# Kernel optimization log

Hardware: AMD Instinct MI355X
Metric: run time of the kernel (lower is better)

## Reference

```python
import jax, jax.numpy as jnp
import numpy as np

T, B, A, H = 1024, 16, 8, 256


def setup_inputs() -> dict:
    key = jax.random.key(0)
    ks = jax.random.split(key, 8)
    s = 1.0 / np.sqrt(H)  # approximate lecun/orthogonal scale for stability
    return {
        "ins": jax.random.normal(ks[0], (T, B, A, H), dtype=jnp.float32),
        "resets": jax.random.randint(ks[1], (T, B, A), 0, 2) == 1,
        "h0": jnp.zeros((B, A, H), dtype=jnp.float32),
        "W_ir": jax.random.normal(ks[2], (H, H), dtype=jnp.float32) * s,
        "W_iz": jax.random.normal(ks[3], (H, H), dtype=jnp.float32) * s,
        "W_in": jax.random.normal(ks[4], (H, H), dtype=jnp.float32) * s,
        "b_ir": jnp.zeros((H,), dtype=jnp.float32),
        "b_iz": jnp.zeros((H,), dtype=jnp.float32),
        "b_in": jnp.zeros((H,), dtype=jnp.float32),
        "W_hr": jax.random.normal(ks[5], (H, H), dtype=jnp.float32) * s,
        "W_hz": jax.random.normal(ks[6], (H, H), dtype=jnp.float32) * s,
        "W_hn": jax.random.normal(ks[7], (H, H), dtype=jnp.float32) * s,
        "b_hn": jnp.zeros((H,), dtype=jnp.float32),
    }


def reference(ins, resets, h0, W_ir, W_iz, W_in, b_ir, b_iz, b_in, W_hr, W_hz, W_hn, b_hn):
    # Precompute the input-side gate projections for all timesteps at once
    # (mathematically identical to flax GRUCell's per-step dense_i calls).
    xr = ins @ W_ir + b_ir  # [T, B, A, H]
    xz = ins @ W_iz + b_iz
    xn = ins @ W_in + b_in

    def step(h, xs):
        xr_t, xz_t, xn_t, rst_t = xs
        # reset masking: re-init carry to zeros where episode resets
        h = jnp.where(rst_t[..., None], jnp.zeros_like(h), h)
        r = jax.nn.sigmoid(xr_t + h @ W_hr)
        z = jax.nn.sigmoid(xz_t + h @ W_hz)
        n = jnp.tanh(xn_t + r * (h @ W_hn + b_hn))
        new_h = (1.0 - z) * n + z * h
        return new_h, new_h

    final_h, ys = jax.lax.scan(step, h0, (xr, xz, xn, resets))
    return ys  # [T, B, A, H]; final carry == ys[-1]
```

## Files before the change

### kernel.cpp

```cpp
#include <hip/hip_runtime.h>

#define BA 128
#define H 256
#define TH 768
#define NROWS (1024 * BA)
#define LCAP 65536
#define NBUCK 8
#define MT 32
#define AP 264

typedef _Float16 h2_t __attribute__((ext_vector_type(2)));
typedef _Float16 h8_t __attribute__((ext_vector_type(8)));
typedef short s8_t __attribute__((ext_vector_type(8)));
typedef float f4_t __attribute__((ext_vector_type(4)));
typedef unsigned short u16;
typedef u16 us4_t __attribute__((ext_vector_type(4)));
typedef unsigned int u32;
typedef u32 v64u __attribute__((ext_vector_type(64)));

__device__ __forceinline__ float bf2f(u16 u) {
  union { u32 i; float f; } c; c.i = ((u32)u) << 16; return c.f;
}
__device__ __forceinline__ u16 f2bf(float f) {
  union { float f; u32 i; } c; c.f = f;
  u32 r = c.i + 0x7FFFu + ((c.i >> 16) & 1u);
  return (u16)(r >> 16);
}
__device__ __forceinline__ float sigm(float x) {
  float e = __builtin_amdgcn_exp2f(-x * 1.442695040888963f);
  return __builtin_amdgcn_rcpf(1.0f + e);
}
__device__ __forceinline__ float tanh_(float x) {
  float e = __builtin_amdgcn_exp2f(x * 2.885390081777927f);
  return 1.0f - 2.0f * __builtin_amdgcn_rcpf(1.0f + e);
}
__device__ __forceinline__ float ldf(const void* p, bool f32, size_t idx) {
  return f32 ? ((const float*)p)[idx] : bf2f(((const u16*)p)[idx]);
}
__device__ __forceinline__ int ldrst(const void* p, bool isbyte, size_t idx) {
  return isbyte ? (int)((const unsigned char*)p)[idx] : ((const int*)p)[idx];
}
__device__ __forceinline__ float F2(h2_t a, h2_t b, float c) {
#if defined(__has_builtin) && __has_builtin(__builtin_amdgcn_fdot2)
  return __builtin_amdgcn_fdot2(a, b, c, false);
#else
  return c + (float)a[0] * (float)b[0] + (float)a[1] * (float)b[1];
#endif
}

__global__ __launch_bounds__(256) void kdetect(const u32* __restrict__ insw,
                                               const u32* __restrict__ rstw,
                                               const u32* __restrict__ whrw,
                                               const u32* __restrict__ wirw,
                                               int* __restrict__ flags,
                                               int* __restrict__ cnt) {
  __shared__ int c0, c1, c2, c3;
  if (threadIdx.x == 0) { c0 = 0; c1 = 0; c2 = 0; c3 = 0; }
  if (threadIdx.x < NBUCK) cnt[threadIdx.x] = 0;
  __syncthreads();
  if (!(fabsf(bf2f((u16)(insw[threadIdx.x] & 0xFFFFu))) < 1e10f)) atomicAdd(&c0, 1);
  if (!(fabsf(bf2f((u16)(whrw[threadIdx.x] & 0xFFFFu))) < 1e10f)) atomicAdd(&c2, 1);
  if (!(fabsf(bf2f((u16)(wirw[threadIdx.x] & 0xFFFFu))) < 1e10f)) atomicAdd(&c3, 1);
  if (threadIdx.x < 128 && rstw[threadIdx.x] > 1u) atomicAdd(&c1, 1);
  __syncthreads();
  if (threadIdx.x == 0) {
    flags[0] = (c0 > 8) ? 1 : 0;
    flags[1] = (c1 > 0) ? 1 : 0;
    flags[2] = (c2 > 8) ? 1 : 0;
    flags[3] = (c3 > 8) ? 1 : 0;
  }
}

__global__ __launch_bounds__(256) void kprep(const void* __restrict__ ins,
                                             u16* __restrict__ insb,
                                             const int* __restrict__ flags) {
  bool f32in = flags[0] != 0;
  size_t i0 = ((size_t)blockIdx.x * 256 + threadIdx.x) * 8;
  s8_t v;
  if (f32in) {
    f4_t x0 = *(const f4_t*)((const float*)ins + i0);
    f4_t x1 = *(const f4_t*)((const float*)ins + i0 + 4);
#pragma unroll
    for (int i = 0; i < 4; ++i) v[i] = (short)f2bf(x0[i]);
#pragma unroll
    for (int i = 0; i < 4; ++i) v[4 + i] = (short)f2bf(x1[i]);
  } else {
    v = *(const s8_t*)((const u16*)ins + i0);
  }
  *(s8_t*)(insb + i0) = v;
}

__global__ __launch_bounds__(256) void ktrans(const void* __restrict__ W0, const void* __restrict__ W1,
                                              const void* __restrict__ W2, const void* __restrict__ W3,
                                              const void* __restrict__ W4, const void* __restrict__ W5,
                                              u16* __restrict__ WT, const int* __restrict__ flags) {
  __shared__ u16 tile[64][65];
  int g = blockIdx.z;
  bool f32in = ((g < 3) ? flags[3] : flags[2]) != 0;
  bool toF16 = (g >= 3);
  const void* srcs[6] = {W0, W1, W2, W3, W4, W5};
  const void* src = srcs[g];
  int k0 = blockIdx.x * 64, j0 = blockIdx.y * 64;
  int tid = threadIdx.x;
#pragma unroll
  for (int p = 0; p < 16; ++p) {
    int e = p * 256 + tid;
    int kr = e >> 6, jc = e & 63;
    size_t idx = (size_t)(k0 + kr) * H + j0 + jc;
    float v = f32in ? ((const float*)src)[idx] : bf2f(((const u16*)src)[idx]);
    u16 bits;
    if (toF16) {
      _Float16 h = (_Float16)v;
      bits = __builtin_bit_cast(u16, h);
    } else {
      bits = f2bf(v);
    }
    tile[kr][jc] = bits;
  }
  __syncthreads();
  u16* dst = WT + (size_t)g * H * H;
#pragma unroll
  for (int p = 0; p < 16; ++p) {
    int e = p * 256 + tid;
    int jr = e >> 6, kc = e & 63;
    dst[(size_t)(j0 + jr) * H + k0 + kc] = tile[kc][jr];
  }
}

__global__ __launch_bounds__(256) void kswz(const u16* __restrict__ WT, u16* __restrict__ WhB) {
  int f = blockIdx.x * 256 + threadIdx.x;
  if (f >= 8 * 48 * 64) return;
  int lane = f & 63;
  int cg = (f >> 6) % 48;
  int kk = (f >> 6) / 48;
  int g = cg >> 4;
  int col = ((cg & 15) << 4) + (lane & 15);
  int k0 = kk * 32 + ((lane >> 4) << 3);
  const u16* src = WT + (size_t)(3 + g) * H * H + (size_t)col * H + k0;
  *(s8_t*)(WhB + (size_t)f * 8) = *(const s8_t*)src;
}

#define LDK 40
__global__ __launch_bounds__(256) void kgemm(const void* __restrict__ ins,
                                             const u16* __restrict__ insb, int use_insb,
                                             int t0, const u16* __restrict__ WT,
                                             u16* __restrict__ C,
                                             const int* __restrict__ flags) {
  __shared__ u16 As[128 * LDK];
  __shared__ u16 Bs[128 * LDK];
  bool f32in = flags[0] != 0;
  int tid = threadIdx.x;
  int row0 = blockIdx.x * 128;
  int col0 = blockIdx.y * 128;
  int gate = col0 >> 8;
  int j0 = col0 & 255;
  const u16* Bg = WT + (size_t)gate * H * H + (size_t)j0 * H;
  size_t abase = (size_t)t0 * BA * H;
  int lane = tid & 63;
  int wave = tid >> 6;
  int r16 = lane & 15;
  int kg = lane >> 4;
  f4_t acc[2][8];
#pragma unroll
  for (int rt = 0; rt < 2; ++rt)
#pragma unroll
    for (int ct = 0; ct < 8; ++ct) acc[rt][ct] = (f4_t)0.0f;

  for (int kk = 0; kk < 8; ++kk) {
    int k0 = kk * 32;
#pragma unroll
    for (int p = 0; p < 2; ++p) {
      int idx = p * 256 + tid;
      int m = idx >> 2;
      int kq = (idx & 3) * 8;
      size_t e = abase + (size_t)(row0 + m) * H + k0 + kq;
      s8_t v;
      if (use_insb) {
        v = *(const s8_t*)(insb + e);
      } else if (f32in) {
        f4_t x0 = *(const f4_t*)((const float*)ins + e);
        f4_t x1 = *(const f4_t*)((const float*)ins + e + 4);
#pragma unroll
        for (int i = 0; i < 4; ++i) v[i] = (short)f2bf(x0[i]);
#pragma unroll
        for (int i = 0; i < 4; ++i) v[4 + i] = (short)f2bf(x1[i]);
      } else {
        v = *(const s8_t*)((const u16*)ins + e);
      }
      *(s8_t*)(As + m * LDK + kq) = v;
    }
#pragma unroll
    for (int p = 0; p < 2; ++p) {
      int idx = p * 256 + tid;
      int n = idx >> 2;
      int kq = (idx & 3) * 8;
      s8_t v = *(const s8_t*)(Bg + (size_t)n * H + k0 + kq);
      *(s8_t*)(Bs + n * LDK + kq) = v;
    }
    __syncthreads();
    s8_t af[2], bf[8];
#pragma unroll
    for (int rt = 0; rt < 2; ++rt)
      af[rt] = *(const s8_t*)(As + (wave * 32 + rt * 16 + r16) * LDK + kg * 8);
#pragma unroll
    for (int ct = 0; ct < 8; ++ct)
      bf[ct] = *(const s8_t*)(Bs + (ct * 16 + r16) * LDK + kg * 8);
#pragma unroll
    for (int rt = 0; rt < 2; ++rt)
#pragma unroll
      for (int ct = 0; ct < 8; ++ct)
        acc[rt][ct] = __builtin_amdgcn_mfma_f32_16x16x32_bf16(af[rt], bf[ct], acc[rt][ct], 0, 0, 0);
    __syncthreads();
  }
#pragma unroll
  for (int rt = 0; rt < 2; ++rt)
#pragma unroll
    for (int ct = 0; ct < 8; ++ct)
#pragma unroll
      for (int r = 0; r < 4; ++r) {
        int grow = row0 + wave * 32 + rt * 16 + kg * 4 + r;
        int gcol = col0 + ct * 16 + r16;
        C[(size_t)grow * TH + gcol] = f2bf(acc[rt][ct][r]);
      }
}

__global__ __launch_bounds__(256) void kdlists(const void* __restrict__ resets,
                                               unsigned char* __restrict__ dbuf,
                                               int* __restrict__ cnt,
                                               u32* __restrict__ list,
                                               const int* __restrict__ flags) {
  bool rbyte = flags[1] != 0;
  int w = blockIdx.x;
  int tid = threadIdx.x;
  __shared__ unsigned char rst[1024];
  __shared__ unsigned char dS[1024];
  __shared__ int lcnt[NBUCK], lbase[NBUCK], lpos[NBUCK];
  if (tid < NBUCK) { lcnt[tid] = 0; lpos[tid] = 0; }
  for (int t = tid; t < 1024; t += 256)
    rst[t] = (unsigned char)(ldrst(resets, rbyte, (size_t)t * BA + w) != 0);
  __syncthreads();
#pragma unroll
  for (int p = 0; p < 4; ++p) {
    int t = p * 256 + tid;
    int d;
    if (rst[t]) {
      d = 255;
    } else {
      int tr = t - 1;
      while (tr >= 0 && !rst[tr]) --tr;
      d = t - ((tr >= 0) ? tr : 0);
      if (d > 254) d = 254;
    }
    dS[t] = (unsigned char)d;
    if (d < NBUCK) atomicAdd(&lcnt[d], 1);
  }
  __syncthreads();
  if (tid < NBUCK) lbase[tid] = atomicAdd(&cnt[tid], lcnt[tid]);
  for (int t = tid; t < 1024; t += 256) dbuf[(size_t)w * 1024 + t] = dS[t];
  __syncthreads();
#pragma unroll
  for (int p = 0; p < 4; ++p) {
    int t = p * 256 + tid;
    int d = dS[t];
    if (d < NBUCK) {
      int pos = lbase[d] + atomicAdd(&lpos[d], 1);
      if (pos < LCAP) list[(size_t)d * LCAP + pos] = (u32)(t * BA + w);
    }
  }
}

__global__ __launch_bounds__(256) void kelem(const u16* __restrict__ xproj,
                                             const void* __restrict__ resets,
                                             float* __restrict__ out,
                                             const void* __restrict__ bir, const void* __restrict__ biz,
                                             const void* __restrict__ bin_, const void* __restrict__ bhn,
                                             const int* __restrict__ flags) {
  bool rbyte = flags[1] != 0;
  bool wf32 = flags[2] != 0;
  int j = threadIdx.x;
  float vbir = ldf(bir, wf32, j), vbiz = ldf(biz, wf32, j);
  float vbin = ldf(bin_, wf32, j), vbhn = ldf(bhn, wf32, j);
  for (int i = blockIdx.x; i < NROWS; i += gridDim.x) {
    if (!ldrst(resets, rbyte, i)) continue;
    size_t xb = (size_t)i * TH + j;
    float r = sigm(bf2f(xproj[xb]) + vbir);
    float z = sigm(bf2f(xproj[xb + H]) + vbiz);
    float n = tanh_(bf2f(xproj[xb + 2 * H]) + vbin + r * vbhn);
    out[(size_t)i * H + j] = (1.0f - z) * n;
  }
}

__global__ __launch_bounds__(512) void kstep(const u16* __restrict__ xproj,
                                             float* __restrict__ out,
                                             const void* __restrict__ h0,
                                             const u16* __restrict__ WhB,
                                             const int* __restrict__ cnt,
                                             const u32* __restrict__ list,
                                             const void* __restrict__ bir, const void* __restrict__ biz,
                                             const void* __restrict__ bin_, const void* __restrict__ bhn,
                                             const int* __restrict__ flags, int s) {
  int cs = cnt[s];
  if (cs <= 0) return;
  bool wf32 = flags[2] != 0;
  __shared__ __align__(16) u16 As[MT * AP];
  __shared__ int ridS[MT];
  int tid = threadIdx.x;
  int lane = tid & 63;
  int wv = tid >> 6;
  int r16 = lane & 15;
  int kg = lane >> 4;
  int ntiles = (cs + MT - 1) / MT;
  float vb[2][4];
#pragma unroll
  for (int jt = 0; jt < 2; ++jt) {
    int j = wv * 32 + jt * 16 + r16;
    vb[jt][0] = ldf(bir, wf32, j);
    vb[jt][1] = ldf(biz, wf32, j);
    vb[jt][2] = ldf(bin_, wf32, j);
    vb[jt][3] = ldf(bhn, wf32, j);
  }
  const s8_t* WB = (const s8_t*)WhB;

  for (int tile = blockIdx.x; tile < ntiles; tile += gridDim.x) {
    __syncthreads();
    {
      int i = tid >> 4;
      int seg = tid & 15;
      int idx = tile * MT + i;
      int rid = (idx < cs) ? (int)list[idx] : -1;
      if (seg == 0) ridS[i] = rid;
      u16* dst = As + i * AP + seg * 16;
      if (rid >= 0) {
        if (s == 0) {
#pragma unroll
          for (int q = 0; q < 4; ++q) {
            us4_t hb;
#pragma unroll
            for (int e = 0; e < 4; ++e) {
              _Float16 hh = (_Float16)ldf(h0, wf32, (size_t)rid * H + seg * 16 + q * 4 + e);
              hb[e] = __builtin_bit_cast(u16, hh);
            }
            *(us4_t*)(dst + q * 4) = hb;
          }
        } else {
          const float* src = out + (size_t)(rid - BA) * H + seg * 16;
#pragma unroll
          for (int q = 0; q < 4; ++q) {
            f4_t v = *(const f4_t*)(src + q * 4);
            us4_t hb;
#pragma unroll
            for (int e = 0; e < 4; ++e) {
              _Float16 hh = (_Float16)v[e];
              hb[e] = __builtin_bit_cast(u16, hh);
            }
            *(us4_t*)(dst + q * 4) = hb;
          }
        }
      } else {
        us4_t hz; hz[0] = 0; hz[1] = 0; hz[2] = 0; hz[3] = 0;
#pragma unroll
        for (int q = 0; q < 4; ++q) *(us4_t*)(dst + q * 4) = hz;
      }
    }
    __syncthreads();

    f4_t acc[2][6];
#pragma unroll
    for (int a = 0; a < 2; ++a)
#pragma unroll
      for (int b = 0; b < 6; ++b) acc[a][b] = (f4_t)0.0f;

#pragma unroll 2
    for (int kk = 0; kk < 8; ++kk) {
      h8_t af[2];
#pragma unroll
      for (int mt = 0; mt < 2; ++mt)
        af[mt] = __builtin_bit_cast(h8_t,
            *(const s8_t*)(As + (mt * 16 + r16) * AP + kk * 32 + kg * 8));
      s8_t bfr[6];
#pragma unroll
      for (int g = 0; g < 3; ++g)
#pragma unroll
        for (int jt = 0; jt < 2; ++jt) {
          int cg = g * 16 + wv * 2 + jt;
          bfr[g * 2 + jt] = WB[(size_t)((kk * 48 + cg) * 64 + lane)];
        }
#pragma unroll
      for (int c = 0; c < 6; ++c)
#pragma unroll
        for (int mt = 0; mt < 2; ++mt)
          acc[mt][c] = __builtin_amdgcn_mfma_f32_16x16x32_f16(
              af[mt], __builtin_bit_cast(h8_t, bfr[c]), acc[mt][c], 0, 0, 0);
    }

#pragma unroll
    for (int mt = 0; mt < 2; ++mt)
#pragma unroll
      for (int r = 0; r < 4; ++r) {
        int rowl = mt * 16 + kg * 4 + r;
        int rid = ridS[rowl];
        if (rid < 0) continue;
#pragma unroll
        for (int jt = 0; jt < 2; ++jt) {
          int j = wv * 32 + jt * 16 + r16;
          size_t xb = (size_t)rid * TH + j;
          float rg = sigm(bf2f(xproj[xb]) + vb[jt][0] + acc[mt][jt][r]);
          float zg = sigm(bf2f(xproj[xb + H]) + vb[jt][1] + acc[mt][2 + jt][r]);
          float ng = tanh_(bf2f(xproj[xb + 2 * H]) + vb[jt][2] + rg * (acc[mt][4 + jt][r] + vb[jt][3]));
          float hp = (s == 0) ? ldf(h0, wf32, (size_t)rid * H + j)
                              : out[(size_t)(rid - BA) * H + j];
          out[(size_t)rid * H + j] = (1.0f - zg) * ng + zg * hp;
        }
      }
  }
}

#define LDW(VR, P, c) { uint4 q_ = *(const uint4*)((P) + (c) * 8); \
  VR[(c)*4+0] = q_.x; VR[(c)*4+1] = q_.y; VR[(c)*4+2] = q_.z; VR[(c)*4+3] = q_.w; }
#define LDWALL(VR, P) \
  LDW(VR,P,0) LDW(VR,P,1) LDW(VR,P,2) LDW(VR,P,3) LDW(VR,P,4) LDW(VR,P,5) LDW(VR,P,6) LDW(VR,P,7) \
  LDW(VR,P,8) LDW(VR,P,9) LDW(VR,P,10) LDW(VR,P,11) LDW(VR,P,12) LDW(VR,P,13) LDW(VR,P,14) LDW(VR,P,15)

#define BCH(x) __builtin_bit_cast(h2_t, (u32)(x))
#define DOTC(c) { uint4 hv_ = h4_[c]; \
  h2_t a0_ = __builtin_bit_cast(h2_t, hv_.x); \
  h2_t a1_ = __builtin_bit_cast(h2_t, hv_.y); \
  h2_t a2_ = __builtin_bit_cast(h2_t, hv_.z); \
  h2_t a3_ = __builtin_bit_cast(h2_t, hv_.w); \
  ar = F2(BCH(WR[4*(c)+0]), a0_, ar); az = F2(BCH(WZ[4*(c)+0]), a0_, az); an = F2(BCH(WN[4*(c)+0]), a0_, an); \
  ar = F2(BCH(WR[4*(c)+1]), a1_, ar); az = F2(BCH(WZ[4*(c)+1]), a1_, az); an = F2(BCH(WN[4*(c)+1]), a1_, an); \
  ar = F2(BCH(WR[4*(c)+2]), a2_, ar); az = F2(BCH(WZ[4*(c)+2]), a2_, az); an = F2(BCH(WN[4*(c)+2]), a2_, an); \
  ar = F2(BCH(WR[4*(c)+3]), a3_, ar); az = F2(BCH(WZ[4*(c)+3]), a3_, az); an = F2(BCH(WN[4*(c)+3]), a3_, an); }
#define DOT16 \
  DOTC(0) DOTC(1) DOTC(2) DOTC(3) DOTC(4) DOTC(5) DOTC(6) DOTC(7) \
  DOTC(8) DOTC(9) DOTC(10) DOTC(11) DOTC(12) DOTC(13) DOTC(14) DOTC(15)

__global__ __launch_bounds__(512, 2) void ktail(const u16* __restrict__ xproj,
                                                float* __restrict__ out,
                                                const u16* __restrict__ WhF,
                                                const unsigned char* __restrict__ dbuf,
                                                const void* __restrict__ bir, const void* __restrict__ biz,
                                                const void* __restrict__ bin_, const void* __restrict__ bhn,
                                                const int* __restrict__ flags) {
  int w = blockIdx.x;
  int tid = threadIdx.x;
  int j = tid >> 1;
  int half = tid & 1;
  bool wf32 = flags[2] != 0;
  __shared__ __align__(16) u16 hsb[256];
  __shared__ unsigned char dcol[1024];
  for (int t = tid; t < 1024; t += 512) dcol[t] = dbuf[(size_t)w * 1024 + t];
  const u16* pr = WhF + (size_t)j * H + half * 128;
  const u16* pz = WhF + (size_t)H * H + (size_t)j * H + half * 128;
  const u16* pn = WhF + (size_t)2 * H * H + (size_t)j * H + half * 128;
  v64u WR, WZ, WN;
  LDWALL(WR, pr)
  LDWALL(WZ, pz)
  LDWALL(WN, pn)
  float vbir = ldf(bir, wf32, j), vbiz = ldf(biz, wf32, j);
  float vbin = ldf(bin_, wf32, j), vbhn = ldf(bhn, wf32, j);
  __syncthreads();
  int prev_t = -99;
  float hreg = 0.0f;
#pragma unroll 1
  for (int t = 0; t < 1024; ++t) {
    int d = dcol[t];
    if (d < NBUCK || d == 255) continue;
    if (prev_t != t - 1) {
      hreg = out[((size_t)(t - 1) * BA + w) * H + j];
      if (half == 0) { _Float16 hh = (_Float16)hreg; hsb[j] = __builtin_bit_cast(u16, hh); }
      __syncthreads();
    }
    const uint4* h4_ = (const uint4*)(&hsb[half * 128]);
    float ar = 0.0f, az = 0.0f, an = 0.0f;
    DOT16
    ar += __shfl_xor(ar, 1, 64);
    az += __shfl_xor(az, 1, 64);
    an += __shfl_xor(an, 1, 64);
    size_t xb = ((size_t)t * BA + w) * TH + j;
    float r = sigm(bf2f(xproj[xb]) + vbir + ar);
    float z = sigm(bf2f(xproj[xb + H]) + vbiz + az);
    float n = tanh_(bf2f(xproj[xb + 2 * H]) + vbin + r * (an + vbhn));
    float hnew = (1.0f - z) * n + z * hreg;
    if (half == 0) out[((size_t)t * BA + w) * H + j] = hnew;
    __syncthreads();
    if (half == 0) { _Float16 hh = (_Float16)hnew; hsb[j] = __builtin_bit_cast(u16, hh); }
    hreg = hnew;
    prev_t = t;
    __syncthreads();
  }
}

__global__ __launch_bounds__(512, 2) void kscan(
    const u16* __restrict__ xproj, const void* __restrict__ resets,
    const void* __restrict__ h0, float* __restrict__ carry,
    const u16* __restrict__ WhF,
    const void* __restrict__ bir, const void* __restrict__ biz, const void* __restrict__ bin_,
    const void* __restrict__ bhn, float* __restrict__ out, int t0, int Tc,
    const int* __restrict__ flags) {
  int w = blockIdx.x;
  int tid = threadIdx.x;
  int j = tid >> 1;
  int half = tid & 1;
  bool wf32 = flags[2] != 0;
  bool rbyte = flags[1] != 0;
  __shared__ __align__(16) u16 hsb[2][256];
  __shared__ int rstS[1024];

  for (int t = tid; t < Tc; t += 512)
    rstS[t] = ldrst(resets, rbyte, (size_t)(t0 + t) * BA + w);

  const u16* pr = WhF + (size_t)j * H + half * 128;
  const u16* pz = WhF + (size_t)H * H + (size_t)j * H + half * 128;
  const u16* pn = WhF + (size_t)2 * H * H + (size_t)j * H + half * 128;
  v64u WR, WZ, WN;
  LDWALL(WR, pr)
  LDWALL(WZ, pz)
  LDWALL(WN, pn)

  float vbir = ldf(bir, wf32, j), vbiz = ldf(biz, wf32, j);
  float vbin = ldf(bin_, wf32, j), vbhn = ldf(bhn, wf32, j);

  float hreg = (t0 == 0) ? ldf(h0, wf32, (size_t)w * H + j) : carry[(size_t)w * H + j];
  __syncthreads();
  if (rstS[0] != 0) hreg = 0.0f;
  if (half == 0) {
    _Float16 hh = (_Float16)hreg;
    hsb[0][j] = __builtin_bit_cast(u16, hh);
  }
  __syncthreads();

  size_t xb0 = (size_t)w * TH + j;
  u16 cxr = xproj[xb0], cxz = xproj[xb0 + H], cxn = xproj[xb0 + 2 * H];

#pragma unroll 1
  for (int tl = 0; tl < Tc; ++tl) {
    u16 nxr = 0, nxz = 0, nxn = 0;
    if (tl + 1 < Tc) {
      size_t nb = ((size_t)(tl + 1) * BA + w) * TH + j;
      nxr = xproj[nb]; nxz = xproj[nb + H]; nxn = xproj[nb + 2 * H];
    }
    const uint4* h4_ = (const uint4*)(&hsb[tl & 1][half * 128]);
    float ar = 0.0f, az = 0.0f, an = 0.0f;
    DOT16
    ar += __shfl_xor(ar, 1, 64);
    az += __shfl_xor(az, 1, 64);
    an += __shfl_xor(an, 1, 64);
    float r = sigm(bf2f(cxr) + vbir + ar);
    float z = sigm(bf2f(cxz) + vbiz + az);
    float n = tanh_(bf2f(cxn) + vbin + r * (an + vbhn));
    float hnew = (1.0f - z) * n + z * hreg;
    if (half == 0) out[((size_t)(t0 + tl) * BA + w) * H + j] = hnew;

    float hnext = hnew;
    if (tl + 1 < Tc && rstS[tl + 1] != 0) hnext = 0.0f;
    if (half == 0) {
      _Float16 hh = (_Float16)hnext;
      hsb[(tl & 1) ^ 1][j] = __builtin_bit_cast(u16, hh);
    }
    hreg = hnext;
    cxr = nxr; cxz = nxz; cxn = nxn;
    __syncthreads();
  }
  if (half == 0) carry[(size_t)w * H + j] = hreg;
}

extern "C" void kernel_launch(void* const* d_in, const int* in_sizes, int n_in,
                              void* d_out, int out_size, void* d_ws, size_t ws_size,
                              hipStream_t stream) {
  const void* ins = d_in[0];
  const void* resets = d_in[1];
  const void* h0 = d_in[2];
  const void* Wir = d_in[3];
  const void* Wiz = d_in[4];
  const void* Win = d_in[5];
  const void* bir = d_in[6];
  const void* biz = d_in[7];
  const void* bin_ = d_in[8];
  const void* Whr = d_in[9];
  const void* Whz = d_in[10];
  const void* Whn = d_in[11];
  const void* bhn = d_in[12];
  float* out = (float*)d_out;

  const size_t off_wt = 256;
  const size_t wt_bytes = (size_t)6 * H * H * 2;
  const size_t off_carry = off_wt + wt_bytes;
  const size_t off_cnt = off_carry + (size_t)BA * H * 4;
  const size_t off_dbuf = off_cnt + 256;
  const size_t off_list = off_dbuf + NROWS;
  const size_t off_whb = off_list + (size_t)NBUCK * LCAP * 4;
  const size_t whb_bytes = (size_t)TH * H * 2;
  const size_t off_insb = off_whb + whb_bytes;
  const size_t insb_bytes = (size_t)1024 * BA * H * 2;
  const size_t chunk_bytes = (size_t)BA * TH * 2;

  int* flags = (int*)d_ws;
  u16* WT = (u16*)((char*)d_ws + off_wt);
  float* carry = (float*)((char*)d_ws + off_carry);
  int* cnt = (int*)((char*)d_ws + off_cnt);
  unsigned char* dbuf = (unsigned char*)((char*)d_ws + off_dbuf);
  u32* list = (u32*)((char*)d_ws + off_list);
  u16* WhB = (u16*)((char*)d_ws + off_whb);
  u16* insb = (u16*)((char*)d_ws + off_insb);

  int use_insb = (ws_size >= off_insb + insb_bytes + (size_t)1024 * chunk_bytes) ? 1 : 0;
  size_t off_xproj = use_insb ? (off_insb + insb_bytes) : off_insb;
  u16* xproj = (u16*)((char*)d_ws + off_xproj);

  kdetect<<<1, 256, 0, stream>>>((const u32*)ins, (const u32*)resets,
                                 (const u32*)Whr, (const u32*)Wir, flags, cnt);
  if (use_insb) kprep<<<16384, 256, 0, stream>>>(ins, insb, flags);
  ktrans<<<dim3(4, 4, 6), 256, 0, stream>>>(Wir, Wiz, Win, Whr, Whz, Whn, WT, flags);
  kswz<<<96, 256, 0, stream>>>(WT, WhB);

  const u16* WhT = WT + (size_t)3 * H * H;
  if (ws_size >= off_xproj + (size_t)1024 * chunk_bytes) {
    kdlists<<<128, 256, 0, stream>>>(resets, dbuf, cnt, list, flags);
    kgemm<<<dim3(1024, 6), 256, 0, stream>>>(ins, insb, use_insb, 0, WT, xproj, flags);
    kelem<<<1024, 256, 0, stream>>>(xproj, resets, out, bir, biz, bin_, bhn, flags);
    for (int s = 0; s < NBUCK; ++s)
      kstep<<<1024, 512, 0, stream>>>(xproj, out, h0, WhB, cnt, list + (size_t)s * LCAP,
                                      bir, biz, bin_, bhn, flags, s);
    ktail<<<128, 512, 0, stream>>>(xproj, out, WhT, dbuf, bir, biz, bin_, bhn, flags);
  } else {
    int Tc = 1024;
    while (Tc > 1 && off_xproj + (size_t)Tc * chunk_bytes > ws_size) Tc >>= 1;
    int nchunks = 1024 / Tc;
    for (int c = 0; c < nchunks; ++c) {
      int t0 = c * Tc;
      kgemm<<<dim3(Tc, 6), 256, 0, stream>>>(ins, insb, use_insb, t0, WT, xproj, flags);
      kscan<<<128, 512, 0, stream>>>(xproj, resets, h0, carry, WhT,
                                     bir, biz, bin_, bhn, out, t0, Tc, flags);
    }
  }
}
```

Measured before the change: 780.0 us.

## Restructure input GEMM to load A tile once and use pre-swizzled weights

Removes the separate input-to-bf16 prep pass. The input projection GEMM now uses one block per timestep: it loads and converts all 128x256 input rows into LDS once, then loops over all 768 output columns. B fragments are read directly from a pre-swizzled MFMA-layout weight buffer in global memory instead of being staged through LDS. This cuts the repeated A reads (previously once per 6 column blocks) and the extra full pass over the input. In exchange it uses large LDS per block (about 66KB), which may lower occupancy, and it relies on cache hits for the B fragment loads.

```diff
diff --git a/kernel.cpp b/kernel.cpp
--- a/kernel.cpp
+++ b/kernel.cpp
@@ -8,6 +8,7 @@
 #define NBUCK 8
 #define MT 32
 #define AP 264
+#define NFRAG (8 * 48 * 64)
 
 typedef _Float16 h2_t __attribute__((ext_vector_type(2)));
 typedef _Float16 h8_t __attribute__((ext_vector_type(8)));
@@ -69,25 +70,6 @@
     flags[2] = (c2 > 8) ? 1 : 0;
     flags[3] = (c3 > 8) ? 1 : 0;
   }
-}
-
-__global__ __launch_bounds__(256) void kprep(const void* __restrict__ ins,
-                                             u16* __restrict__ insb,
-                                             const int* __restrict__ flags) {
-  bool f32in = flags[0] != 0;
-  size_t i0 = ((size_t)blockIdx.x * 256 + threadIdx.x) * 8;
-  s8_t v;
-  if (f32in) {
-    f4_t x0 = *(const f4_t*)((const float*)ins + i0);
-    f4_t x1 = *(const f4_t*)((const float*)ins + i0 + 4);
-#pragma unroll
-    for (int i = 0; i < 4; ++i) v[i] = (short)f2bf(x0[i]);
-#pragma unroll
-    for (int i = 0; i < 4; ++i) v[4 + i] = (short)f2bf(x1[i]);
-  } else {
-    v = *(const s8_t*)((const u16*)ins + i0);
-  }
-  *(s8_t*)(insb + i0) = v;
 }
 
 __global__ __launch_bounds__(256) void ktrans(const void* __restrict__ W0, const void* __restrict__ W1,
@@ -127,101 +109,94 @@
   }
 }
 
-__global__ __launch_bounds__(256) void kswz(const u16* __restrict__ WT, u16* __restrict__ WhB) {
-  int f = blockIdx.x * 256 + threadIdx.x;
-  if (f >= 8 * 48 * 64) return;
-  int lane = f & 63;
-  int cg = (f >> 6) % 48;
-  int kk = (f >> 6) / 48;
-  int g = cg >> 4;
+__global__ __launch_bounds__(256) void kswz(const u16* __restrict__ WT, u16* __restrict__ WB) {
+  int fl = blockIdx.x * 256 + threadIdx.x;
+  if (fl >= NFRAG) return;
+  int part = blockIdx.y;
+  int lane = fl & 63;
+  int cg = (fl >> 6) % 48;
+  int kk = (fl >> 6) / 48;
+  int g = part * 3 + (cg >> 4);
   int col = ((cg & 15) << 4) + (lane & 15);
   int k0 = kk * 32 + ((lane >> 4) << 3);
-  const u16* src = WT + (size_t)(3 + g) * H * H + (size_t)col * H + k0;
-  *(s8_t*)(WhB + (size_t)f * 8) = *(const s8_t*)src;
-}
-
-#define LDK 40
+  const u16* src = WT + (size_t)g * H * H + (size_t)col * H + k0;
+  *(s8_t*)(WB + ((size_t)part * NFRAG + fl) * 8) = *(const s8_t*)src;
+}
+
 __global__ __launch_bounds__(256) void kgemm(const void* __restrict__ ins,
-                                             const u16* __restrict__ insb, int use_insb,
-                                             int t0, const u16* __restrict__ WT,
+                                             int t0, const u16* __restrict__ WiB,
                                              u16* __restrict__ C,
                                              const int* __restrict__ flags) {
-  __shared__ u16 As[128 * LDK];
-  __shared__ u16 Bs[128 * LDK];
+  __shared__ __align__(16) u16 As[128 * AP];
   bool f32in = flags[0] != 0;
   int tid = threadIdx.x;
-  int row0 = blockIdx.x * 128;
-  int col0 = blockIdx.y * 128;
-  int gate = col0 >> 8;
-  int j0 = col0 & 255;
-  const u16* Bg = WT + (size_t)gate * H * H + (size_t)j0 * H;
-  size_t abase = (size_t)t0 * BA * H;
+  int bt = blockIdx.x;
+  size_t abase = (size_t)(t0 + bt) * BA * H;
+#pragma unroll
+  for (int q = 0; q < 16; ++q) {
+    int idx = q * 256 + tid;
+    int row = idx >> 5;
+    int col0 = (idx & 31) * 8;
+    s8_t v;
+    if (f32in) {
+      const float* s = (const float*)ins + abase + (size_t)idx * 8;
+      f4_t x0 = *(const f4_t*)s;
+      f4_t x1 = *(const f4_t*)(s + 4);
+#pragma unroll
+      for (int i = 0; i < 4; ++i) v[i] = (short)f2bf(x0[i]);
+#pragma unroll
+      for (int i = 0; i < 4; ++i) v[4 + i] = (short)f2bf(x1[i]);
+    } else {
+      v = *(const s8_t*)((const u16*)ins + abase + (size_t)idx * 8);
+    }
+    *(s8_t*)(As + row * AP + col0) = v;
+  }
+  __syncthreads();
+
   int lane = tid & 63;
-  int wave = tid >> 6;
+  int wv = tid >> 6;
+  int wr = wv >> 1;
+  int wc = wv & 1;
   int r16 = lane & 15;
   int kg = lane >> 4;
-  f4_t acc[2][8];
-#pragma unroll
-  for (int rt = 0; rt < 2; ++rt)
-#pragma unroll
-    for (int ct = 0; ct < 8; ++ct) acc[rt][ct] = (f4_t)0.0f;
-
-  for (int kk = 0; kk < 8; ++kk) {
-    int k0 = kk * 32;
-#pragma unroll
-    for (int p = 0; p < 2; ++p) {
-      int idx = p * 256 + tid;
-      int m = idx >> 2;
-      int kq = (idx & 3) * 8;
-      size_t e = abase + (size_t)(row0 + m) * H + k0 + kq;
-      s8_t v;
-      if (use_insb) {
-        v = *(const s8_t*)(insb + e);
-      } else if (f32in) {
-        f4_t x0 = *(const f4_t*)((const float*)ins + e);
-        f4_t x1 = *(const f4_t*)((const float*)ins + e + 4);
-#pragma unroll
-        for (int i = 0; i < 4; ++i) v[i] = (short)f2bf(x0[i]);
-#pragma unroll
-        for (int i = 0; i < 4; ++i) v[4 + i] = (short)f2bf(x1[i]);
-      } else {
-        v = *(const s8_t*)((const u16*)ins + e);
+  const s8_t* WB = (const s8_t*)WiB;
+  int row0 = bt * 128;
+
+  for (int c = 0; c < 6; ++c) {
+    f4_t acc[4][4];
+#pragma unroll
+    for (int a = 0; a < 4; ++a)
+#pragma unroll
+      for (int b = 0; b < 4; ++b) acc[a][b] = (f4_t)0.0f;
+#pragma unroll 2
+    for (int kk = 0; kk < 8; ++kk) {
+      s8_t af[4];
+#pragma unroll
+      for (int mt = 0; mt < 4; ++mt)
+        af[mt] = *(const s8_t*)(As + (wr * 64 + mt * 16 + r16) * AP + kk * 32 + kg * 8);
+      s8_t bfr[4];
+#pragma unroll
+      for (int ct = 0; ct < 4; ++ct) {
+        int cg = c * 8 + wc * 4 + ct;
+        bfr[ct] = WB[(size_t)((kk * 48 + cg) * 64 + lane)];
       }
-      *(s8_t*)(As + m * LDK + kq) = v;
-    }
-#pragma unroll
-    for (int p = 0; p < 2; ++p) {
-      int idx = p * 256 + tid;
-      int n = idx >> 2;
-      int kq = (idx & 3) * 8;
-      s8_t v = *(const s8_t*)(Bg + (size_t)n * H + k0 + kq);
-      *(s8_t*)(Bs + n * LDK + kq) = v;
-    }
-    __syncthreads();
-    s8_t af[2], bf[8];
-#pragma unroll
-    for (int rt = 0; rt < 2; ++rt)
-      af[rt] = *(const s8_t*)(As + (wave * 32 + rt * 16 + r16) * LDK + kg * 8);
-#pragma unroll
-    for (int ct = 0; ct < 8; ++ct)
-      bf[ct] = *(const s8_t*)(Bs + (ct * 16 + r16) * LDK + kg * 8);
-#pragma unroll
-    for (int rt = 0; rt < 2; ++rt)
-#pragma unroll
-      for (int ct = 0; ct < 8; ++ct)
-        acc[rt][ct] = __builtin_amdgcn_mfma_f32_16x16x32_bf16(af[rt], bf[ct], acc[rt][ct], 0, 0, 0);
-    __syncthreads();
-  }
-#pragma unroll
-  for (int rt = 0; rt < 2; ++rt)
-#pragma unroll
-    for (int ct = 0; ct < 8; ++ct)
-#pragma unroll
-      for (int r = 0; r < 4; ++r) {
-        int grow = row0 + wave * 32 + rt * 16 + kg * 4 + r;
-        int gcol = col0 + ct * 16 + r16;
-        C[(size_t)grow * TH + gcol] = f2bf(acc[rt][ct][r]);
-      }
+#pragma unroll
+      for (int ct = 0; ct < 4; ++ct)
+#pragma unroll
+        for (int mt = 0; mt < 4; ++mt)
+          acc[mt][ct] = __builtin_amdgcn_mfma_f32_16x16x32_bf16(af[mt], bfr[ct], acc[mt][ct], 0, 0, 0);
+    }
+#pragma unroll
+    for (int mt = 0; mt < 4; ++mt)
+#pragma unroll
+      for (int ct = 0; ct < 4; ++ct)
+#pragma unroll
+        for (int r = 0; r < 4; ++r) {
+          int grow = row0 + wr * 64 + mt * 16 + kg * 4 + r;
+          int gcol = c * 128 + wc * 64 + ct * 16 + r16;
+          C[(size_t)grow * TH + gcol] = f2bf(acc[mt][ct][r]);
+        }
+  }
 }
 
 __global__ __launch_bounds__(256) void kdlists(const void* __restrict__ resets,
@@ -589,10 +564,9 @@
   const size_t off_cnt = off_carry + (size_t)BA * H * 4;
   const size_t off_dbuf = off_cnt + 256;
   const size_t off_list = off_dbuf + NROWS;
-  const size_t off_whb = off_list + (size_t)NBUCK * LCAP * 4;
-  const size_t whb_bytes = (size_t)TH * H * 2;
-  const size_t off_insb = off_whb + whb_bytes;
-  const size_t insb_bytes = (size_t)1024 * BA * H * 2;
+  const size_t off_wb = off_list + (size_t)NBUCK * LCAP * 4;
+  const size_t wb_bytes = (size_t)2 * TH * H * 2;
+  const size_t off_xproj = off_wb + wb_bytes;
   const size_t chunk_bytes = (size_t)BA * TH * 2;
 
   int* flags = (int*)d_ws;
@@ -601,23 +575,20 @@
   int* cnt = (int*)((char*)d_ws + off_cnt);
   unsigned char* dbuf = (unsigned char*)((char*)d_ws + off_dbuf);
   u32* list = (u32*)((char*)d_ws + off_list);
-  u16* WhB = (u16*)((char*)d_ws + off_whb);
-  u16* insb = (u16*)((char*)d_ws + off_insb);
-
-  int use_insb = (ws_size >= off_insb + insb_bytes + (size_t)1024 * chunk_bytes) ? 1 : 0;
-  size_t off_xproj = use_insb ? (off_insb + insb_bytes) : off_insb;
+  u16* WB = (u16*)((char*)d_ws + off_wb);
   u16* xproj = (u16*)((char*)d_ws + off_xproj);
 
   kdetect<<<1, 256, 0, stream>>>((const u32*)ins, (const u32*)resets,
                                  (const u32*)Whr, (const u32*)Wir, flags, cnt);
-  if (use_insb) kprep<<<16384, 256, 0, stream>>>(ins, insb, flags);
   ktrans<<<dim3(4, 4, 6), 256, 0, stream>>>(Wir, Wiz, Win, Whr, Whz, Whn, WT, flags);
-  kswz<<<96, 256, 0, stream>>>(WT, WhB);
-
+  kswz<<<dim3(96, 2), 256, 0, stream>>>(WT, WB);
+
+  const u16* WiB = WB;
+  const u16* WhB = WB + (size_t)NFRAG * 8;
   const u16* WhT = WT + (size_t)3 * H * H;
   if (ws_size >= off_xproj + (size_t)1024 * chunk_bytes) {
     kdlists<<<128, 256, 0, stream>>>(resets, dbuf, cnt, list, flags);
-    kgemm<<<dim3(1024, 6), 256, 0, stream>>>(ins, insb, use_insb, 0, WT, xproj, flags);
+    kgemm<<<1024, 256, 0, stream>>>(ins, 0, WiB, xproj, flags);
     kelem<<<1024, 256, 0, stream>>>(xproj, resets, out, bir, biz, bin_, bhn, flags);
     for (int s = 0; s < NBUCK; ++s)
       kstep<<<1024, 512, 0, stream>>>(xproj, out, h0, WhB, cnt, list + (size_t)s * LCAP,
@@ -629,7 +600,7 @@
     int nchunks = 1024 / Tc;
     for (int c = 0; c < nchunks; ++c) {
       int t0 = c * Tc;
-      kgemm<<<dim3(Tc, 6), 256, 0, stream>>>(ins, insb, use_insb, t0, WT, xproj, flags);
+      kgemm<<<Tc, 256, 0, stream>>>(ins, t0, WiB, xproj, flags);
       kscan<<<128, 512, 0, stream>>>(xproj, resets, h0, carry, WhT,
                                      bir, biz, bin_, bhn, out, t0, Tc, flags);
     }
```

After: 731.3 us. 6.2% less time.
